# Performance work log

Measured on AMD Instinct MI355X. Metric: run time of the kernel, lower is better.

## Reference

```python
import jax, jax.numpy as jnp
import numpy as np

N_NODES = 50000
N_EDGES = 800000
D_IN = 64
D_OUT = 64


def setup_inputs() -> dict:
    key = jax.random.key(0)
    k1, k2, k3, k4, k5, k6 = jax.random.split(key, 6)
    feat = jax.random.normal(k1, (N_NODES, D_IN), dtype=jnp.float32)
    edge_weight = jax.random.uniform(k2, (N_EDGES, 1), dtype=jnp.float32)
    # xavier_uniform bound for [D_IN, D_OUT]
    bound = float(np.sqrt(6.0 / (D_IN + D_OUT)))
    W1 = jax.random.uniform(k3, (D_IN, D_OUT), minval=-bound, maxval=bound, dtype=jnp.float32)
    W2 = jax.random.uniform(k4, (D_IN, D_OUT), minval=-bound, maxval=bound, dtype=jnp.float32)
    src = jax.random.randint(k5, (N_EDGES,), 0, N_NODES, dtype=jnp.int64)
    dst = jax.random.randint(k6, (N_EDGES,), 0, N_NODES, dtype=jnp.int64)
    return {"feat": feat, "edge_weight": edge_weight, "W1": W1, "W2": W2, "src": src, "dst": dst}


def reference(feat, edge_weight, W1, W2, src, dst):
    # message: u_sub_e -> src feature minus (broadcast) edge weight  [E, D_IN]
    msgs = feat[src] - edge_weight
    # sum aggregation over destination nodes  [N, D_IN]
    agg = jax.ops.segment_sum(msgs, dst, num_segments=feat.shape[0])
    # dual dense projections; no activation (activation=None)
    rst = jnp.matmul(feat, W1) + jnp.matmul(agg, W2)
    return rst
```

## Files before the change

kernel.cpp:

```cpp
#include <hip/hip_runtime.h>

#define NN 50000
#define NE 800000
#define D  64
#define NB 782
#define EBLK 2048
#define NEB 391
#define CAPB 1280
#define CONVB 1563

typedef unsigned int u32;
typedef unsigned short u16;
typedef unsigned long long u64;
typedef __attribute__((ext_vector_type(8))) short bf16x8;
typedef __attribute__((ext_vector_type(4))) float f32x4;
typedef __attribute__((ext_vector_type(2))) float f32x2;

__device__ __forceinline__ int wave_incl_scan(int v, int lane) {
    #pragma unroll
    for (int off = 1; off < 64; off <<= 1) {
        int t = __shfl_up(v, off);
        if (lane >= off) v += t;
    }
    return v;
}

__device__ __forceinline__ u32 f2bf(float x) {
    u32 u = __float_as_uint(x);
    return (u + 0x7fffu + ((u >> 16) & 1u)) >> 16;
}

__device__ __forceinline__ bf16x8 as_bf8(uint4 u) {
    union { uint4 a; bf16x8 b; } x; x.a = u; return x.b;
}

__device__ __forceinline__ u32 pk_fp8x4(float a, float b, float c, float d) {
    int w = __builtin_amdgcn_cvt_pk_fp8_f32(a, b, 0, false);
    w = __builtin_amdgcn_cvt_pk_fp8_f32(c, d, w, true);
    return (u32)w;
}

__global__ __launch_bounds__(256) void convz_kernel(const float* __restrict__ feat,
                                                    uint4* __restrict__ featb,
                                                    uint2* __restrict__ featb8,
                                                    u32* __restrict__ cursor)
{
    int tid = threadIdx.x;
    if (blockIdx.x == CONVB) {
        for (int i = tid; i < NB; i += 256) cursor[i] = 0;
        return;
    }
    int i = blockIdx.x * 256 + tid;
    if (i >= NN * D / 8) return;
    const float4* f4 = (const float4*)feat;
    float4 a = f4[2 * i], b = f4[2 * i + 1];
    uint4 o;
    o.x = f2bf(a.x) | (f2bf(a.y) << 16);
    o.y = f2bf(a.z) | (f2bf(a.w) << 16);
    o.z = f2bf(b.x) | (f2bf(b.y) << 16);
    o.w = f2bf(b.z) | (f2bf(b.w) << 16);
    featb[i] = o;
    uint2 p8;
    p8.x = pk_fp8x4(a.x, a.y, a.z, a.w);
    p8.y = pk_fp8x4(b.x, b.y, b.z, b.w);
    featb8[i] = p8;
}

__global__ __launch_bounds__(256) void kb_scatter(const int* __restrict__ src,
                                                  const int* __restrict__ dst,
                                                  const float* __restrict__ ew,
                                                  u32* __restrict__ cursor,
                                                  u64* __restrict__ sorted)
{
    __shared__ u32 h[NB], eb[NB], ctr[NB], gb[NB];
    __shared__ u64 buf[EBLK];
    int tid = threadIdx.x;
    for (int i = tid; i < NB; i += 256) h[i] = 0;
    __syncthreads();
    int base = blockIdx.x * EBLK;
    int n = min(EBLK, NE - base);
    for (int k = tid; k < n; k += 256)
        atomicAdd(&h[((u32)dst[base + k]) >> 6], 1u);
    __syncthreads();
    if (tid < 64) {
        u32 carry = 0;
        for (int c = 0; c < 13; ++c) {
            int idx = c * 64 + tid;
            u32 v = (idx < NB) ? h[idx] : 0;
            int incl = wave_incl_scan((int)v, tid);
            if (idx < NB) { u32 e = (u32)incl - v + carry; eb[idx] = e; ctr[idx] = e; }
            carry += (u32)__shfl(incl, 63);
        }
    }
    __syncthreads();
    for (int i = tid; i < NB; i += 256) gb[i] = atomicAdd(&cursor[i], h[i]);
    __syncthreads();
    for (int k = tid; k < n; k += 256) {
        int e = base + k;
        u32 d = (u32)dst[e], s = (u32)src[e];
        u64 rec = ((u64)((d << 16) | s) << 32) | (u64)__float_as_uint(ew[e]);
        u32 p = atomicAdd(&ctr[d >> 6], 1u);
        buf[p] = rec;
    }
    __syncthreads();
    for (int k = tid; k < n; k += 256) {
        u64 rec = buf[k];
        u32 bin = (u32)(rec >> 54);
        u32 idx = gb[bin] + (u32)k - eb[bin];
        if (idx < CAPB) sorted[(size_t)bin * CAPB + idx] = rec;
    }
}

__global__ __launch_bounds__(256) void kc_nodesort(const u64* __restrict__ sorted,
                                                   const u32* __restrict__ cursor,
                                                   u16* __restrict__ srcs16,
                                                   u32* __restrict__ nodeStart2,
                                                   float* __restrict__ sW)
{
    __shared__ u32 hcnt[64], hbase[65], ctr[64];
    __shared__ u64 buf[CAPB];
    int tid = threadIdx.x;
    int bin = blockIdx.x;
    int n = min((int)cursor[bin], CAPB);
    const size_t rbase = (size_t)bin * CAPB;

    if (tid < 64) hcnt[tid] = 0;
    __syncthreads();
    for (int k = tid; k < n; k += 256)
        atomicAdd(&hcnt[(int)(sorted[rbase + k] >> 48) & 63], 1u);
    __syncthreads();
    if (tid < 64) {
        u32 v = hcnt[tid];
        int incl = wave_incl_scan((int)v, tid);
        u32 ex = (u32)incl - v;
        hbase[tid] = ex; ctr[tid] = ex;
        if (tid == 63) hbase[64] = (u32)incl;
    }
    __syncthreads();
    for (int k = tid; k < n; k += 256) {
        u64 rec = sorted[rbase + k];
        u32 p = atomicAdd(&ctr[(int)(rec >> 48) & 63], 1u);
        buf[p] = rec;
    }
    __syncthreads();
    for (int k = tid; k < n; k += 256)
        srcs16[rbase + k] = (u16)(buf[k] >> 32);
    if (tid < 64) {
        nodeStart2[bin * 65 + tid] = (u32)rbase + hbase[tid];
        if (tid == 0) nodeStart2[bin * 65 + 64] = (u32)rbase + hbase[64];
        int node = (bin << 6) + tid;
        if (node < NN) {
            float s = 0.f;
            for (int j = (int)hbase[tid]; j < (int)hbase[tid + 1]; ++j)
                s += __uint_as_float((u32)buf[j]);
            sW[node] = s;
        }
    }
}

__global__ __launch_bounds__(256) void k4_gather(const u32* __restrict__ fb8,
                                                 const u16* __restrict__ srcs16,
                                                 const u32* __restrict__ nodeStart2,
                                                 uint2* __restrict__ aggb)
{
    int wv   = (blockIdx.x * 256 + threadIdx.x) >> 6;
    int lane = threadIdx.x & 63;
    int g    = lane >> 4;
    int li   = lane & 15;
    int node = wv * 4 + g;
    if (node >= NN) return;
    int bin = node >> 6, ln = node & 63;

    int e   = (int)nodeStart2[bin * 65 + ln];
    int end = (int)nodeStart2[bin * 65 + ln + 1];

    float4 acc = make_float4(0.f, 0.f, 0.f, 0.f);
    for (; e + 7 < end; e += 8) {
        int s0 = srcs16[e],     s1 = srcs16[e + 1];
        int s2 = srcs16[e + 2], s3 = srcs16[e + 3];
        int s4 = srcs16[e + 4], s5 = srcs16[e + 5];
        int s6 = srcs16[e + 6], s7 = srcs16[e + 7];
        u32 u0 = fb8[(size_t)s0 * 16 + li];
        u32 u1 = fb8[(size_t)s1 * 16 + li];
        u32 u2 = fb8[(size_t)s2 * 16 + li];
        u32 u3 = fb8[(size_t)s3 * 16 + li];
        u32 u4 = fb8[(size_t)s4 * 16 + li];
        u32 u5 = fb8[(size_t)s5 * 16 + li];
        u32 u6 = fb8[(size_t)s6 * 16 + li];
        u32 u7 = fb8[(size_t)s7 * 16 + li];
        #pragma unroll
        for (int j = 0; j < 8; ++j) {
            u32 uu = j == 0 ? u0 : j == 1 ? u1 : j == 2 ? u2 : j == 3 ? u3
                   : j == 4 ? u4 : j == 5 ? u5 : j == 6 ? u6 : u7;
            f32x2 lo = __builtin_amdgcn_cvt_pk_f32_fp8((int)uu, false);
            f32x2 hi = __builtin_amdgcn_cvt_pk_f32_fp8((int)uu, true);
            acc.x += lo.x; acc.y += lo.y; acc.z += hi.x; acc.w += hi.y;
        }
    }
    for (; e < end; ++e) {
        u32 uu = fb8[(size_t)srcs16[e] * 16 + li];
        f32x2 lo = __builtin_amdgcn_cvt_pk_f32_fp8((int)uu, false);
        f32x2 hi = __builtin_amdgcn_cvt_pk_f32_fp8((int)uu, true);
        acc.x += lo.x; acc.y += lo.y; acc.z += hi.x; acc.w += hi.y;
    }

    uint2 o;
    o.x = f2bf(acc.x) | (f2bf(acc.y) << 16);
    o.y = f2bf(acc.z) | (f2bf(acc.w) << 16);
    aggb[(size_t)node * 16 + li] = o;
}

__global__ __launch_bounds__(256) void gemm_mfma(
    const uint4* __restrict__ featb,
    const uint4* __restrict__ aggb,
    const float* __restrict__ sW,
    const float* __restrict__ W1,
    const float* __restrict__ W2,
    float* __restrict__ out)
{
    __shared__ u16 wT[64][136];
    __shared__ float csp[4][64];
    __shared__ float csum[64];
    const int tid = threadIdx.x;

    for (int i = tid; i < 8192; i += 256) {
        int k = i >> 6, c = i & 63;
        float v = (k < 64) ? W1[i] : W2[i - 4096];
        wT[c][k] = (u16)f2bf(v);
    }
    {
        int c = tid & 63, kq = tid >> 6;
        float s = 0.f;
        for (int k = kq * 16; k < kq * 16 + 16; ++k) s += W2[k * 64 + c];
        csp[kq][c] = s;
    }
    __syncthreads();
    if (tid < 64) csum[tid] = csp[0][tid] + csp[1][tid] + csp[2][tid] + csp[3][tid];
    __syncthreads();

    int gw = blockIdx.x * 4 + (tid >> 6);
    if (gw >= NN / 16) return;
    const int l  = tid & 63;
    const int lr = l & 15;
    const int q  = l >> 4;

    bf16x8 b[4][4];
    #pragma unroll
    for (int nt = 0; nt < 4; ++nt)
        #pragma unroll
        for (int kk = 0; kk < 4; ++kk)
            b[nt][kk] = *(const bf16x8*)&wT[nt * 16 + lr][kk * 32 + q * 8];

    const int m0 = gw * 16;
    const size_t arow = (size_t)(m0 + lr) * 8;
    bf16x8 a0 = as_bf8(featb[arow + q]);
    bf16x8 a1 = as_bf8(featb[arow + 4 + q]);
    bf16x8 a2 = as_bf8(aggb[arow + q]);
    bf16x8 a3 = as_bf8(aggb[arow + 4 + q]);

    f32x4 acc0 = {0.f, 0.f, 0.f, 0.f};
    f32x4 acc1 = acc0, acc2 = acc0, acc3 = acc0;

    acc0 = __builtin_amdgcn_mfma_f32_16x16x32_bf16(a0, b[0][0], acc0, 0, 0, 0);
    acc1 = __builtin_amdgcn_mfma_f32_16x16x32_bf16(a0, b[1][0], acc1, 0, 0, 0);
    acc2 = __builtin_amdgcn_mfma_f32_16x16x32_bf16(a0, b[2][0], acc2, 0, 0, 0);
    acc3 = __builtin_amdgcn_mfma_f32_16x16x32_bf16(a0, b[3][0], acc3, 0, 0, 0);

    acc0 = __builtin_amdgcn_mfma_f32_16x16x32_bf16(a1, b[0][1], acc0, 0, 0, 0);
    acc1 = __builtin_amdgcn_mfma_f32_16x16x32_bf16(a1, b[1][1], acc1, 0, 0, 0);
    acc2 = __builtin_amdgcn_mfma_f32_16x16x32_bf16(a1, b[2][1], acc2, 0, 0, 0);
    acc3 = __builtin_amdgcn_mfma_f32_16x16x32_bf16(a1, b[3][1], acc3, 0, 0, 0);

    acc0 = __builtin_amdgcn_mfma_f32_16x16x32_bf16(a2, b[0][2], acc0, 0, 0, 0);
    acc1 = __builtin_amdgcn_mfma_f32_16x16x32_bf16(a2, b[1][2], acc1, 0, 0, 0);
    acc2 = __builtin_amdgcn_mfma_f32_16x16x32_bf16(a2, b[2][2], acc2, 0, 0, 0);
    acc3 = __builtin_amdgcn_mfma_f32_16x16x32_bf16(a2, b[3][2], acc3, 0, 0, 0);

    acc0 = __builtin_amdgcn_mfma_f32_16x16x32_bf16(a3, b[0][3], acc0, 0, 0, 0);
    acc1 = __builtin_amdgcn_mfma_f32_16x16x32_bf16(a3, b[1][3], acc1, 0, 0, 0);
    acc2 = __builtin_amdgcn_mfma_f32_16x16x32_bf16(a3, b[2][3], acc2, 0, 0, 0);
    acc3 = __builtin_amdgcn_mfma_f32_16x16x32_bf16(a3, b[3][3], acc3, 0, 0, 0);

    float4 sw4 = *(const float4*)&sW[m0 + q * 4];
    const float* swp = (const float*)&sw4;

    #pragma unroll
    for (int r = 0; r < 4; ++r) {
        size_t rowoff = (size_t)(m0 + q * 4 + r) * D;
        float s = swp[r];
        out[rowoff +  0 + lr] = acc0[r] - s * csum[ 0 + lr];
        out[rowoff + 16 + lr] = acc1[r] - s * csum[16 + lr];
        out[rowoff + 32 + lr] = acc2[r] - s * csum[32 + lr];
        out[rowoff + 48 + lr] = acc3[r] - s * csum[48 + lr];
    }
}

extern "C" void kernel_launch(void* const* d_in, const int* in_sizes, int n_in,
                              void* d_out, int out_size, void* d_ws, size_t ws_size,
                              hipStream_t stream)
{
    const float* feat = (const float*)d_in[0];
    const float* ew   = (const float*)d_in[1];
    const float* W1   = (const float*)d_in[2];
    const float* W2   = (const float*)d_in[3];
    const int*   src  = (const int*)  d_in[4];
    const int*   dst  = (const int*)  d_in[5];
    float* out = (float*)d_out;

    char* p = (char*)d_ws;
    size_t o = 0;
    auto take = [&](size_t bytes) { char* q = p + o; o = (o + bytes + 255) & ~(size_t)255; return q; };
    u64* sorted     = (u64*)take((size_t)NB * CAPB * 8);
    u16* srcs16     = (u16*)take((size_t)NB * CAPB * 2);
    u32* cursor     = (u32*)take((size_t)NB * 4);
    u32* nodeStart2 = (u32*)take((size_t)NB * 65 * 4);
    uint4* featb    = (uint4*)take((size_t)NN * D * 2);
    uint2* featb8   = (uint2*)take((size_t)NN * D);
    uint4* aggb     = (uint4*)take((size_t)NN * D * 2);
    float* sW       = (float*)take((size_t)NN * 4 + 256);

    convz_kernel<<<CONVB + 1, 256, 0, stream>>>(feat, featb, featb8, cursor);
    kb_scatter  <<<NEB, 256, 0, stream>>>(src, dst, ew, cursor, sorted);
    kc_nodesort <<<NB, 256, 0, stream>>>(sorted, cursor, srcs16, nodeStart2, sW);
    k4_gather   <<<(NN + 15) / 16, 256, 0, stream>>>((const u32*)featb8, srcs16,
                                                     nodeStart2, (uint2*)aggb);
    gemm_mfma   <<<(NN / 16 + 3) / 4, 256, 0, stream>>>(featb, aggb, sW, W1, W2, out);
}
```

Baseline: 62.47 us.

## Fuse feature conversion into node-sort kernel and compact sorted edge records

The feature bf16/fp8 conversion now runs in extra blocks of the node-sort kernel, and the separate conversion kernel is gone. Zeroing the cursor moves to hipMemsetAsync. Sorted edge records shrink from 64-bit to a 32-bit dst-local/src word plus a 16-bit bf16 edge weight, which cuts scatter and sort traffic and shared memory. The price is that edge-weight sums are now accumulated from bf16-rounded weights, which lowers precision.

```diff
diff --git a/kernel.cpp b/kernel.cpp
--- a/kernel.cpp
+++ b/kernel.cpp
@@ -40,37 +40,12 @@
     return (u32)w;
 }
 
-__global__ __launch_bounds__(256) void convz_kernel(const float* __restrict__ feat,
-                                                    uint4* __restrict__ featb,
-                                                    uint2* __restrict__ featb8,
-                                                    u32* __restrict__ cursor)
-{
-    int tid = threadIdx.x;
-    if (blockIdx.x == CONVB) {
-        for (int i = tid; i < NB; i += 256) cursor[i] = 0;
-        return;
-    }
-    int i = blockIdx.x * 256 + tid;
-    if (i >= NN * D / 8) return;
-    const float4* f4 = (const float4*)feat;
-    float4 a = f4[2 * i], b = f4[2 * i + 1];
-    uint4 o;
-    o.x = f2bf(a.x) | (f2bf(a.y) << 16);
-    o.y = f2bf(a.z) | (f2bf(a.w) << 16);
-    o.z = f2bf(b.x) | (f2bf(b.y) << 16);
-    o.w = f2bf(b.z) | (f2bf(b.w) << 16);
-    featb[i] = o;
-    uint2 p8;
-    p8.x = pk_fp8x4(a.x, a.y, a.z, a.w);
-    p8.y = pk_fp8x4(b.x, b.y, b.z, b.w);
-    featb8[i] = p8;
-}
-
 __global__ __launch_bounds__(256) void kb_scatter(const int* __restrict__ src,
                                                   const int* __restrict__ dst,
                                                   const float* __restrict__ ew,
                                                   u32* __restrict__ cursor,
-                                                  u64* __restrict__ sorted)
+                                                  u32* __restrict__ sortedR,
+                                                  u16* __restrict__ sortedW)
 {
     __shared__ u32 h[NB], eb[NB], ctr[NB], gb[NB];
     __shared__ u64 buf[EBLK];
@@ -98,28 +73,56 @@
     for (int k = tid; k < n; k += 256) {
         int e = base + k;
         u32 d = (u32)dst[e], s = (u32)src[e];
-        u64 rec = ((u64)((d << 16) | s) << 32) | (u64)__float_as_uint(ew[e]);
+        u64 rec = ((u64)d << 32) | ((u64)s << 16) | (u64)f2bf(ew[e]);
         u32 p = atomicAdd(&ctr[d >> 6], 1u);
         buf[p] = rec;
     }
     __syncthreads();
     for (int k = tid; k < n; k += 256) {
         u64 rec = buf[k];
-        u32 bin = (u32)(rec >> 54);
+        u32 bin = (u32)(rec >> 38);
         u32 idx = gb[bin] + (u32)k - eb[bin];
-        if (idx < CAPB) sorted[(size_t)bin * CAPB + idx] = rec;
-    }
-}
-
-__global__ __launch_bounds__(256) void kc_nodesort(const u64* __restrict__ sorted,
-                                                   const u32* __restrict__ cursor,
-                                                   u16* __restrict__ srcs16,
-                                                   u32* __restrict__ nodeStart2,
-                                                   float* __restrict__ sW)
+        if (idx < CAPB) {
+            u32 dstl = (u32)(rec >> 32) & 63u;
+            u32 s    = (u32)(rec >> 16) & 0xffffu;
+            sortedR[(size_t)bin * CAPB + idx] = (dstl << 16) | s;
+            sortedW[(size_t)bin * CAPB + idx] = (u16)(rec & 0xffffu);
+        }
+    }
+}
+
+__global__ __launch_bounds__(256) void kc_conv(const u32* __restrict__ sortedR,
+                                               const u16* __restrict__ sortedW,
+                                               const u32* __restrict__ cursor,
+                                               const float* __restrict__ feat,
+                                               u16* __restrict__ srcs16,
+                                               u32* __restrict__ nodeStart2,
+                                               float* __restrict__ sW,
+                                               uint4* __restrict__ featb,
+                                               uint2* __restrict__ featb8)
 {
     __shared__ u32 hcnt[64], hbase[65], ctr[64];
-    __shared__ u64 buf[CAPB];
+    __shared__ u16 bufR[CAPB], bufW[CAPB];
     int tid = threadIdx.x;
+
+    if (blockIdx.x >= NB) {
+        int i = (blockIdx.x - NB) * 256 + tid;
+        if (i >= NN * D / 8) return;
+        const float4* f4 = (const float4*)feat;
+        float4 a = f4[2 * i], b = f4[2 * i + 1];
+        uint4 o;
+        o.x = f2bf(a.x) | (f2bf(a.y) << 16);
+        o.y = f2bf(a.z) | (f2bf(a.w) << 16);
+        o.z = f2bf(b.x) | (f2bf(b.y) << 16);
+        o.w = f2bf(b.z) | (f2bf(b.w) << 16);
+        featb[i] = o;
+        uint2 p8;
+        p8.x = pk_fp8x4(a.x, a.y, a.z, a.w);
+        p8.y = pk_fp8x4(b.x, b.y, b.z, b.w);
+        featb8[i] = p8;
+        return;
+    }
+
     int bin = blockIdx.x;
     int n = min((int)cursor[bin], CAPB);
     const size_t rbase = (size_t)bin * CAPB;
@@ -127,7 +130,7 @@
     if (tid < 64) hcnt[tid] = 0;
     __syncthreads();
     for (int k = tid; k < n; k += 256)
-        atomicAdd(&hcnt[(int)(sorted[rbase + k] >> 48) & 63], 1u);
+        atomicAdd(&hcnt[(sortedR[rbase + k] >> 16) & 63u], 1u);
     __syncthreads();
     if (tid < 64) {
         u32 v = hcnt[tid];
@@ -138,13 +141,15 @@
     }
     __syncthreads();
     for (int k = tid; k < n; k += 256) {
-        u64 rec = sorted[rbase + k];
-        u32 p = atomicAdd(&ctr[(int)(rec >> 48) & 63], 1u);
-        buf[p] = rec;
+        u32 r = sortedR[rbase + k];
+        u16 w = sortedW[rbase + k];
+        u32 p = atomicAdd(&ctr[(r >> 16) & 63u], 1u);
+        bufR[p] = (u16)(r & 0xffffu);
+        bufW[p] = w;
     }
     __syncthreads();
     for (int k = tid; k < n; k += 256)
-        srcs16[rbase + k] = (u16)(buf[k] >> 32);
+        srcs16[rbase + k] = bufR[k];
     if (tid < 64) {
         nodeStart2[bin * 65 + tid] = (u32)rbase + hbase[tid];
         if (tid == 0) nodeStart2[bin * 65 + 64] = (u32)rbase + hbase[64];
@@ -152,7 +157,7 @@
         if (node < NN) {
             float s = 0.f;
             for (int j = (int)hbase[tid]; j < (int)hbase[tid + 1]; ++j)
-                s += __uint_as_float((u32)buf[j]);
+                s += __uint_as_float((u32)bufW[j] << 16);
             sW[node] = s;
         }
     }
@@ -310,7 +315,8 @@
     char* p = (char*)d_ws;
     size_t o = 0;
     auto take = [&](size_t bytes) { char* q = p + o; o = (o + bytes + 255) & ~(size_t)255; return q; };
-    u64* sorted     = (u64*)take((size_t)NB * CAPB * 8);
+    u32* sortedR    = (u32*)take((size_t)NB * CAPB * 4);
+    u16* sortedW    = (u16*)take((size_t)NB * CAPB * 2);
     u16* srcs16     = (u16*)take((size_t)NB * CAPB * 2);
     u32* cursor     = (u32*)take((size_t)NB * 4);
     u32* nodeStart2 = (u32*)take((size_t)NB * 65 * 4);
@@ -319,10 +325,11 @@
     uint4* aggb     = (uint4*)take((size_t)NN * D * 2);
     float* sW       = (float*)take((size_t)NN * 4 + 256);
 
-    convz_kernel<<<CONVB + 1, 256, 0, stream>>>(feat, featb, featb8, cursor);
-    kb_scatter  <<<NEB, 256, 0, stream>>>(src, dst, ew, cursor, sorted);
-    kc_nodesort <<<NB, 256, 0, stream>>>(sorted, cursor, srcs16, nodeStart2, sW);
-    k4_gather   <<<(NN + 15) / 16, 256, 0, stream>>>((const u32*)featb8, srcs16,
-                                                     nodeStart2, (uint2*)aggb);
-    gemm_mfma   <<<(NN / 16 + 3) / 4, 256, 0, stream>>>(featb, aggb, sW, W1, W2, out);
-}
+    hipMemsetAsync(cursor, 0, (size_t)NB * 4, stream);
+    kb_scatter<<<NEB, 256, 0, stream>>>(src, dst, ew, cursor, sortedR, sortedW);
+    kc_conv   <<<NB + CONVB, 256, 0, stream>>>(sortedR, sortedW, cursor, feat,
+                                               srcs16, nodeStart2, sW, featb, featb8);
+    k4_gather <<<(NN + 15) / 16, 256, 0, stream>>>((const u32*)featb8, srcs16,
+                                                   nodeStart2, (uint2*)aggb);
+    gemm_mfma <<<(NN / 16 + 3) / 4, 256, 0, stream>>>(featb, aggb, sW, W1, W2, out);
+}
```

After: 67.05 us. +7.3%, slower.
